# Optimization experiments

Measured on AMD Instinct MI355X. Metric: run time of the kernel, lower is better.

The kernel has to match this reference:

```python
import jax, jax.numpy as jnp
import numpy as np

B, L, D, V, O = 512, 256, 256, 100000, 1000  # L must equal D (see MaxPool1d(kernel_size=D) + squeeze)


def setup_inputs() -> dict:
    key = jax.random.key(0)
    k1, k2, k3, k4, k5 = jax.random.split(key, 5)
    input_sentence = jax.random.randint(k1, (B, L), 0, V)
    emb_weight = jax.random.normal(k2, (V, D), dtype=jnp.float32) * 0.02
    # xavier_uniform for W_b: bound = sqrt(6/(D+D))
    bound = float(np.sqrt(6.0 / (D + D)))
    W_b = jax.random.uniform(k3, (D, D), dtype=jnp.float32, minval=-bound, maxval=bound)
    lw = float(np.sqrt(1.0 / D))
    lin_w = jax.random.uniform(k4, (O, D), dtype=jnp.float32, minval=-lw, maxval=lw)
    lin_b = jax.random.uniform(k5, (O,), dtype=jnp.float32, minval=-lw, maxval=lw)
    return {"input_sentence": input_sentence, "emb_weight": emb_weight,
            "W_b": W_b, "lin_w": lin_w, "lin_b": lin_b}


def reference(input_sentence, emb_weight, W_b, lin_w, lin_b):
    # Embedding lookup: [B, L, D]
    we = emb_weight[input_sentence]
    # torch stores embeddings as [B, D, L] then re-transposes inside the co-attention;
    # net effect: C = tanh(E W_b E^T) with E = [B, L, D]  ->  C: [B, L, L]
    C = jnp.tanh(jnp.einsum('bld,de,bme->blm', we, W_b, we))
    # Dropout(p=0.5) is identity in eval mode.
    # MaxPool1d(kernel_size=D) over last axis with L == D -> max over last dim, keepdims
    max_cow = jnp.max(C, axis=-1, keepdims=True)          # [B, L, 1]
    a_q = jax.nn.softmax(max_cow, axis=1)                  # softmax over L
    # bmm(a_q^T [B,1,L], E [B,L,D]) -> [B,1,D], then squeeze dim 1
    f_w = jnp.einsum('blo,bld->bod', a_q, we)[:, 0, :]     # [B, D]
    return f_w @ lin_w.T + lin_b                           # [B, O]
```

## Files before the change

### kernel.cpp

```cpp
#include <hip/hip_runtime.h>
#include <hip/hip_bf16.h>
#include <math.h>

#define B_ 512
#define L_ 256
#define D_ 256
#define V_ 100000
#define O_ 1000

typedef __attribute__((ext_vector_type(8))) short short8;
typedef __attribute__((ext_vector_type(4))) float f32x4;

static __device__ __forceinline__ unsigned short f2bf(float f) {
    union { float f; unsigned u; } v; v.f = f;
    unsigned r = v.u + 0x7FFFu + ((v.u >> 16) & 1u);
    return (unsigned short)(r >> 16);
}
static __device__ __forceinline__ float bf2f(unsigned short u) {
    union { unsigned u; float f; } v; v.u = ((unsigned)u) << 16;
    return v.f;
}
static __device__ __forceinline__ short8 pack8(float4 a, float4 c) {
    short8 o;
    o[0] = (short)f2bf(a.x); o[1] = (short)f2bf(a.y);
    o[2] = (short)f2bf(a.z); o[3] = (short)f2bf(a.w);
    o[4] = (short)f2bf(c.x); o[5] = (short)f2bf(c.y);
    o[6] = (short)f2bf(c.z); o[7] = (short)f2bf(c.w);
    return o;
}
static __device__ __forceinline__ int fsw(int d) { return d ^ (((d >> 5) & 7) << 2); }

__global__ __launch_bounds__(256) void k_wt(const float* __restrict__ Wb,
                                            unsigned short* __restrict__ Wbf) {
    int i = blockIdx.x * 256 + threadIdx.x;
    Wbf[i] = f2bf(Wb[i]);
}

__global__ __launch_bounds__(512) void k_attn(const int* __restrict__ tok,
                                              const float* __restrict__ emb,
                                              const unsigned short* __restrict__ Wbf,
                                              float* __restrict__ fw) {
    __shared__ __align__(16) char lds[163840];
    char* EsC = lds;
    float* red2    = (float*)(lds + 131072);
    float* scratch = (float*)(lds + 132096);
    float* fred    = (float*)(lds + 132160);

    int b = blockIdx.x;
    int tid = threadIdx.x;
    int wid = tid >> 6, ln = tid & 63;
    int l16 = ln & 15, gp = ln >> 4;
    bool prod = (wid < 4);
    int i0 = (prod ? wid : (wid - 4)) * 64;
    const int* tb = tok + (b << 8);

#pragma unroll
    for (int it = 0; it < 4; it++) {
        int c = it * 512 + tid;
        int row = c >> 5, c16 = c & 31;
        const float4* src = (const float4*)(emb + ((size_t)tb[row] << 8) + (c16 << 3));
        short8 o = pack8(src[0], src[1]);
        *(short8*)(EsC + ((row << 9) | ((c16 << 4) ^ ((row & 7) << 4)))) = o;
    }
    __syncthreads();

    short8 afr[8][4];
    if (prod) {
#pragma unroll
        for (int k = 0; k < 8; k++)
#pragma unroll
            for (int rf = 0; rf < 4; rf++)
                afr[k][rf] = *(const short8*)(Wbf + ((i0 + rf * 16 + l16) << 8) + k * 32 + gp * 8);
    }

    float rmax[16];
#pragma unroll
    for (int i = 0; i < 16; i++) rmax[i] = -1e30f;

    auto P2body = [&](char* HtR) {
        f32x4 acc[4][2] = {};
#pragma unroll
        for (int k0 = 0; k0 < 256; k0 += 32) {
            int kk2 = (k0 + gp * 8) * 2;
            short8 b2[2];
#pragma unroll
            for (int cf = 0; cf < 2; cf++) {
                int m = cf * 16 + l16;
                b2[cf] = *(const short8*)(HtR + ((m << 9) | (kk2 ^ ((m & 7) << 4))));
            }
            int ks = k0 >> 5;
            __builtin_amdgcn_s_setprio(1);
#pragma unroll
            for (int rf = 0; rf < 4; rf++)
#pragma unroll
                for (int cf = 0; cf < 2; cf++)
                    acc[rf][cf] = __builtin_amdgcn_mfma_f32_16x16x32_bf16(
                        afr[ks][rf], b2[cf], acc[rf][cf], 0, 0, 0);
            __builtin_amdgcn_s_setprio(0);
        }
#pragma unroll
        for (int rf = 0; rf < 4; rf++)
#pragma unroll
            for (int r = 0; r < 4; r++)
                rmax[rf * 4 + r] = fmaxf(rmax[rf * 4 + r],
                                         fmaxf(acc[rf][0][r], acc[rf][1][r]));
    };

    for (int s = 0; s < 8; s++) {
        if (prod) {
            char* HtW = lds + 131072 + ((s & 1) << 14);
            f32x4 acc[4][2] = {};
#pragma unroll
            for (int k0 = 0; k0 < 256; k0 += 32) {
                int kk2 = (k0 + gp * 8) * 2;
                short8 b1[2];
#pragma unroll
                for (int cf = 0; cf < 2; cf++) {
                    int jg = s * 32 + cf * 16 + l16;
                    b1[cf] = *(const short8*)(EsC + ((jg << 9) | (kk2 ^ ((jg & 7) << 4))));
                }
                int ks = k0 >> 5;
                __builtin_amdgcn_s_setprio(1);
#pragma unroll
                for (int rf = 0; rf < 4; rf++)
#pragma unroll
                    for (int cf = 0; cf < 2; cf++)
                        acc[rf][cf] = __builtin_amdgcn_mfma_f32_16x16x32_bf16(
                            afr[ks][rf], b1[cf], acc[rf][cf], 0, 0, 0);
                __builtin_amdgcn_s_setprio(0);
            }
#pragma unroll
            for (int rf = 0; rf < 4; rf++)
#pragma unroll
                for (int cf = 0; cf < 2; cf++) {
                    int i = i0 + rf * 16 + gp * 4;
                    int jl = cf * 16 + l16;
                    unsigned long long pk;
                    unsigned short* p = (unsigned short*)&pk;
                    p[0] = f2bf(acc[rf][cf][0]);
                    p[1] = f2bf(acc[rf][cf][1]);
                    p[2] = f2bf(acc[rf][cf][2]);
                    p[3] = f2bf(acc[rf][cf][3]);
                    *(unsigned long long*)(HtW + ((jl << 9) | ((i * 2) ^ ((jl & 7) << 4)))) = pk;
                }
        } else {
            if (s == 0) {
                if (wid > 4) {
#pragma unroll 4
                    for (int it = 0; it < 32; it++) {
                        int ch = it * 64 + ln;
                        int rl = ch >> 5, c16 = ch & 31;
                        int row = i0 + rl;
                        const float4* src = (const float4*)(emb + ((size_t)tb[row] << 8) + (c16 << 3));
                        short8 o = pack8(src[0], src[1]);
                        *(short8*)(EsC + ((row << 9) | ((c16 << 4) ^ ((row & 7) << 4)))) = o;
                    }
                }
#pragma unroll
                for (int k = 0; k < 8; k++)
#pragma unroll
                    for (int rf = 0; rf < 4; rf++) {
                        int l = i0 + rf * 16 + l16;
                        afr[k][rf] = *(const short8*)(EsC +
                            ((l << 9) | ((k * 64 + gp * 16) ^ ((l & 7) << 4))));
                    }
            } else {
                P2body(lds + 131072 + (((s - 1) & 1) << 14));
            }
        }
        __syncthreads();
    }

    if (!prod) {
        P2body(lds + 131072 + (1 << 14));
#pragma unroll
        for (int i = 0; i < 16; i++) {
            float v = rmax[i];
            v = fmaxf(v, __shfl_xor(v, 1));
            v = fmaxf(v, __shfl_xor(v, 2));
            v = fmaxf(v, __shfl_xor(v, 4));
            v = fmaxf(v, __shfl_xor(v, 8));
            rmax[i] = v;
        }
        if (l16 == 0) {
#pragma unroll
            for (int rf = 0; rf < 4; rf++)
#pragma unroll
                for (int r = 0; r < 4; r++)
                    red2[i0 + rf * 16 + gp * 4 + r] = rmax[rf * 4 + r];
        }
    }
    __syncthreads();

    float x = -1e30f;
    if (tid < 256) x = tanhf(red2[tid]);
    float mx = x;
#pragma unroll
    for (int s = 1; s < 64; s <<= 1) mx = fmaxf(mx, __shfl_xor(mx, s));
    if (ln == 0) scratch[wid] = mx;
    __syncthreads();
    float bm = scratch[0];
#pragma unroll
    for (int i = 1; i < 8; i++) bm = fmaxf(bm, scratch[i]);
    float e = (tid < 256) ? expf(x - bm) : 0.f;
    float sm = e;
#pragma unroll
    for (int s = 1; s < 64; s <<= 1) sm += __shfl_xor(sm, s);
    if (ln == 0) scratch[8 + wid] = sm;
    __syncthreads();
    float tot = 0.f;
#pragma unroll
    for (int i = 0; i < 8; i++) tot += scratch[8 + i];
    if (tid < 256) red2[tid] = e / tot;
    __syncthreads();

    {
        int g = tid >> 5;
        int d0 = (tid & 31) << 3;
        float s0[8] = {0.f, 0.f, 0.f, 0.f, 0.f, 0.f, 0.f, 0.f};
        int lbase = g << 4;
#pragma unroll
        for (int li = 0; li < 16; li++) {
            int l = lbase + li;
            float aql = red2[l];
            int byt = (l << 9) | ((d0 * 2) ^ ((l & 7) << 4));
            short8 v = *(const short8*)(EsC + byt);
#pragma unroll
            for (int jj = 0; jj < 8; jj++)
                s0[jj] += aql * bf2f((unsigned short)v[jj]);
        }
        f32x4 w0, w1;
        w0[0] = s0[0]; w0[1] = s0[1]; w0[2] = s0[2]; w0[3] = s0[3];
        w1[0] = s0[4]; w1[1] = s0[5]; w1[2] = s0[6]; w1[3] = s0[7];
        *(f32x4*)(fred + g * 256 + fsw(d0)) = w0;
        *(f32x4*)(fred + g * 256 + fsw(d0 + 4)) = w1;
    }
    __syncthreads();
    if (tid < 256) {
        float f = 0.f;
        int dw = fsw(tid);
#pragma unroll
        for (int g2 = 0; g2 < 16; g2++) f += fred[g2 * 256 + dw];
        fw[(b << 8) + tid] = f;
    }
}

__global__ __launch_bounds__(256) void k_out(const float* __restrict__ fw,
                                             const float* __restrict__ lw,
                                             const float* __restrict__ lb,
                                             float* __restrict__ out) {
    __shared__ float BsT[256][68];
    __shared__ float As[32][260];
    int tid = threadIdx.x;
    int tx = tid & 15, ty = tid >> 4;
    int r0 = blockIdx.y * 32, n0 = blockIdx.x * 64;
#pragma unroll
    for (int it = 0; it < 8; it++) {
        int f4 = it * 256 + tid;
        int i = f4 >> 6, kc = (f4 & 63) << 2;
        *(float4*)&As[i][kc] = *(const float4*)&fw[(r0 + i) * 256 + kc];
    }
#pragma unroll
    for (int it = 0; it < 16; it++) {
        int f4 = it * 256 + tid;
        int n = f4 >> 6, kc = (f4 & 63) << 2;
        int nn = n0 + n;
        float4 v = {0.f, 0.f, 0.f, 0.f};
        if (nn < O_) v = *(const float4*)&lw[(size_t)nn * 256 + kc];
        BsT[kc][n] = v.x; BsT[kc + 1][n] = v.y; BsT[kc + 2][n] = v.z; BsT[kc + 3][n] = v.w;
    }
    __syncthreads();
    float acc[2][4] = {};
#pragma unroll 4
    for (int k = 0; k < 256; k++) {
        float4 bv = *(const float4*)&BsT[k][tx * 4];
        float a0 = As[ty * 2][k], a1 = As[ty * 2 + 1][k];
        acc[0][0] += a0 * bv.x; acc[0][1] += a0 * bv.y; acc[0][2] += a0 * bv.z; acc[0][3] += a0 * bv.w;
        acc[1][0] += a1 * bv.x; acc[1][1] += a1 * bv.y; acc[1][2] += a1 * bv.z; acc[1][3] += a1 * bv.w;
    }
#pragma unroll
    for (int i = 0; i < 2; i++)
#pragma unroll
        for (int j = 0; j < 4; j++) {
            int n = n0 + tx * 4 + j;
            if (n < O_) out[(size_t)(r0 + ty * 2 + i) * O_ + n] = acc[i][j] + lb[n];
        }
}

extern "C" void kernel_launch(void* const* d_in, const int* in_sizes, int n_in,
                              void* d_out, int out_size, void* d_ws, size_t ws_size,
                              hipStream_t stream) {
    const int* tok = (const int*)d_in[0];
    const float* emb = (const float*)d_in[1];
    const float* Wb = (const float*)d_in[2];
    const float* lw = (const float*)d_in[3];
    const float* lb = (const float*)d_in[4];
    float* out = (float*)d_out;

    char* ws = (char*)d_ws;
    unsigned short* Wbf = (unsigned short*)(ws);
    float*          fwp = (float*)(ws + 131072);

    hipLaunchKernelGGL(k_wt,   dim3(256),    dim3(256), 0, stream, Wb, Wbf);
    hipLaunchKernelGGL(k_attn, dim3(512),    dim3(512), 0, stream, tok, emb, Wbf, fwp);
    hipLaunchKernelGGL(k_out,  dim3(16, 16), dim3(256), 0, stream, fwp, lw, lb, out);
}
```

Measured before the change: 79.22 us.

## Restructure attention GEMMs with 32x32 MFMA and register-resident intermediate

Replaces the producer/consumer warp split, which staged the intermediate E·W product through double-buffered LDS, with a scheme where each warp computes its own 32 rows of the intermediate using 32x32x16 MFMAs. The result is converted to bf16 with a packed convert instruction and rearranged across lanes via shuffles so it feeds the second GEMM directly from registers. W_b is pre-transposed and read straight from global/L2 per k-step, and LDS use is trimmed so two blocks can fit per CU. The risks are higher register pressure from the 8 f32x16 accumulators plus 16 B fragments, and repeated global reads of W_b.

```diff
diff --git a/kernel.cpp b/kernel.cpp
--- a/kernel.cpp
+++ b/kernel.cpp
@@ -10,6 +10,7 @@
 
 typedef __attribute__((ext_vector_type(8))) short short8;
 typedef __attribute__((ext_vector_type(4))) float f32x4;
+typedef __attribute__((ext_vector_type(16))) float f32x16;
 
 static __device__ __forceinline__ unsigned short f2bf(float f) {
     union { float f; unsigned u; } v; v.f = f;
@@ -28,19 +29,25 @@
     o[6] = (short)f2bf(c.z); o[7] = (short)f2bf(c.w);
     return o;
 }
+static __device__ __forceinline__ unsigned cvtpk(float lo, float hi) {
+    unsigned r;
+    asm("v_cvt_pk_bf16_f32 %0, %1, %2" : "=v"(r) : "v"(lo), "v"(hi));
+    return r;
+}
 static __device__ __forceinline__ int fsw(int d) { return d ^ (((d >> 5) & 7) << 2); }
 
-__global__ __launch_bounds__(256) void k_wt(const float* __restrict__ Wb,
-                                            unsigned short* __restrict__ Wbf) {
+__global__ __launch_bounds__(256) void k_wtT(const float* __restrict__ Wb,
+                                             unsigned short* __restrict__ Wbt) {
     int i = blockIdx.x * 256 + threadIdx.x;
-    Wbf[i] = f2bf(Wb[i]);
-}
-
-__global__ __launch_bounds__(512) void k_attn(const int* __restrict__ tok,
-                                              const float* __restrict__ emb,
-                                              const unsigned short* __restrict__ Wbf,
-                                              float* __restrict__ fw) {
-    __shared__ __align__(16) char lds[163840];
+    int e = i >> 8, d = i & 255;
+    Wbt[i] = f2bf(Wb[d * 256 + e]);
+}
+
+__global__ __launch_bounds__(512, 2) void k_attn(const int* __restrict__ tok,
+                                                 const float* __restrict__ emb,
+                                                 const unsigned short* __restrict__ Wbt,
+                                                 float* __restrict__ fw) {
+    __shared__ __align__(16) char lds[148544];
     char* EsC = lds;
     float* red2    = (float*)(lds + 131072);
     float* scratch = (float*)(lds + 132096);
@@ -49,147 +56,76 @@
     int b = blockIdx.x;
     int tid = threadIdx.x;
     int wid = tid >> 6, ln = tid & 63;
-    int l16 = ln & 15, gp = ln >> 4;
-    bool prod = (wid < 4);
-    int i0 = (prod ? wid : (wid - 4)) * 64;
+    int l32 = ln & 31, hi = ln >> 5;
+    int r0 = wid << 5;
     const int* tb = tok + (b << 8);
 
-#pragma unroll
-    for (int it = 0; it < 4; it++) {
-        int c = it * 512 + tid;
-        int row = c >> 5, c16 = c & 31;
+#pragma unroll 4
+    for (int it = 0; it < 16; it++) {
+        int g = it * 64 + ln;
+        int row = r0 + (g >> 5), c16 = g & 31;
         const float4* src = (const float4*)(emb + ((size_t)tb[row] << 8) + (c16 << 3));
         short8 o = pack8(src[0], src[1]);
-        *(short8*)(EsC + ((row << 9) | ((c16 << 4) ^ ((row & 7) << 4)))) = o;
-    }
-    __syncthreads();
-
-    short8 afr[8][4];
-    if (prod) {
-#pragma unroll
-        for (int k = 0; k < 8; k++)
-#pragma unroll
-            for (int rf = 0; rf < 4; rf++)
-                afr[k][rf] = *(const short8*)(Wbf + ((i0 + rf * 16 + l16) << 8) + k * 32 + gp * 8);
-    }
-
-    float rmax[16];
-#pragma unroll
-    for (int i = 0; i < 16; i++) rmax[i] = -1e30f;
-
-    auto P2body = [&](char* HtR) {
-        f32x4 acc[4][2] = {};
-#pragma unroll
-        for (int k0 = 0; k0 < 256; k0 += 32) {
-            int kk2 = (k0 + gp * 8) * 2;
-            short8 b2[2];
-#pragma unroll
-            for (int cf = 0; cf < 2; cf++) {
-                int m = cf * 16 + l16;
-                b2[cf] = *(const short8*)(HtR + ((m << 9) | (kk2 ^ ((m & 7) << 4))));
+        *(short8*)(EsC + ((row << 9) | ((c16 << 4) ^ ((row & 15) << 4)))) = o;
+    }
+
+    f32x16 acc1[8] = {};
+    {
+        int rr = r0 + l32;
+        int rsw = (rr & 15) << 4;
+#pragma unroll 2
+        for (int ks = 0; ks < 16; ks++) {
+            short8 b1 = *(const short8*)(EsC +
+                ((rr << 9) | (((ks << 5) + (hi << 4)) ^ rsw)));
+#pragma unroll
+            for (int t = 0; t < 8; t++) {
+                short8 a = *(const short8*)(Wbt + (((t << 5) + l32) << 8) + (ks << 4) + (hi << 3));
+                acc1[t] = __builtin_amdgcn_mfma_f32_32x32x16_bf16(a, b1, acc1[t], 0, 0, 0);
             }
-            int ks = k0 >> 5;
-            __builtin_amdgcn_s_setprio(1);
-#pragma unroll
-            for (int rf = 0; rf < 4; rf++)
-#pragma unroll
-                for (int cf = 0; cf < 2; cf++)
-                    acc[rf][cf] = __builtin_amdgcn_mfma_f32_16x16x32_bf16(
-                        afr[ks][rf], b2[cf], acc[rf][cf], 0, 0, 0);
-            __builtin_amdgcn_s_setprio(0);
-        }
-#pragma unroll
-        for (int rf = 0; rf < 4; rf++)
-#pragma unroll
-            for (int r = 0; r < 4; r++)
-                rmax[rf * 4 + r] = fmaxf(rmax[rf * 4 + r],
-                                         fmaxf(acc[rf][0][r], acc[rf][1][r]));
-    };
-
-    for (int s = 0; s < 8; s++) {
-        if (prod) {
-            char* HtW = lds + 131072 + ((s & 1) << 14);
-            f32x4 acc[4][2] = {};
-#pragma unroll
-            for (int k0 = 0; k0 < 256; k0 += 32) {
-                int kk2 = (k0 + gp * 8) * 2;
-                short8 b1[2];
-#pragma unroll
-                for (int cf = 0; cf < 2; cf++) {
-                    int jg = s * 32 + cf * 16 + l16;
-                    b1[cf] = *(const short8*)(EsC + ((jg << 9) | (kk2 ^ ((jg & 7) << 4))));
-                }
-                int ks = k0 >> 5;
-                __builtin_amdgcn_s_setprio(1);
-#pragma unroll
-                for (int rf = 0; rf < 4; rf++)
-#pragma unroll
-                    for (int cf = 0; cf < 2; cf++)
-                        acc[rf][cf] = __builtin_amdgcn_mfma_f32_16x16x32_bf16(
-                            afr[ks][rf], b1[cf], acc[rf][cf], 0, 0, 0);
-                __builtin_amdgcn_s_setprio(0);
-            }
-#pragma unroll
-            for (int rf = 0; rf < 4; rf++)
-#pragma unroll
-                for (int cf = 0; cf < 2; cf++) {
-                    int i = i0 + rf * 16 + gp * 4;
-                    int jl = cf * 16 + l16;
-                    unsigned long long pk;
-                    unsigned short* p = (unsigned short*)&pk;
-                    p[0] = f2bf(acc[rf][cf][0]);
-                    p[1] = f2bf(acc[rf][cf][1]);
-                    p[2] = f2bf(acc[rf][cf][2]);
-                    p[3] = f2bf(acc[rf][cf][3]);
-                    *(unsigned long long*)(HtW + ((jl << 9) | ((i * 2) ^ ((jl & 7) << 4)))) = pk;
-                }
-        } else {
-            if (s == 0) {
-                if (wid > 4) {
-#pragma unroll 4
-                    for (int it = 0; it < 32; it++) {
-                        int ch = it * 64 + ln;
-                        int rl = ch >> 5, c16 = ch & 31;
-                        int row = i0 + rl;
-                        const float4* src = (const float4*)(emb + ((size_t)tb[row] << 8) + (c16 << 3));
-                        short8 o = pack8(src[0], src[1]);
-                        *(short8*)(EsC + ((row << 9) | ((c16 << 4) ^ ((row & 7) << 4)))) = o;
-                    }
-                }
-#pragma unroll
-                for (int k = 0; k < 8; k++)
-#pragma unroll
-                    for (int rf = 0; rf < 4; rf++) {
-                        int l = i0 + rf * 16 + l16;
-                        afr[k][rf] = *(const short8*)(EsC +
-                            ((l << 9) | ((k * 64 + gp * 16) ^ ((l & 7) << 4))));
-                    }
-            } else {
-                P2body(lds + 131072 + (((s - 1) & 1) << 14));
-            }
-        }
-        __syncthreads();
-    }
-
-    if (!prod) {
-        P2body(lds + 131072 + (1 << 14));
-#pragma unroll
-        for (int i = 0; i < 16; i++) {
-            float v = rmax[i];
-            v = fmaxf(v, __shfl_xor(v, 1));
-            v = fmaxf(v, __shfl_xor(v, 2));
-            v = fmaxf(v, __shfl_xor(v, 4));
-            v = fmaxf(v, __shfl_xor(v, 8));
-            rmax[i] = v;
-        }
-        if (l16 == 0) {
-#pragma unroll
-            for (int rf = 0; rf < 4; rf++)
-#pragma unroll
-                for (int r = 0; r < 4; r++)
-                    red2[i0 + rf * 16 + gp * 4 + r] = rmax[rf * 4 + r];
-        }
-    }
+        }
+    }
+
+    short8 b2[16];
+#pragma unroll
+    for (int ks = 0; ks < 16; ks++) {
+        int t = ks >> 1, base = (ks & 1) << 3;
+        unsigned u0 = cvtpk(acc1[t][base + 0], acc1[t][base + 1]);
+        unsigned u1 = cvtpk(acc1[t][base + 2], acc1[t][base + 3]);
+        unsigned u2 = cvtpk(acc1[t][base + 4], acc1[t][base + 5]);
+        unsigned u3 = cvtpk(acc1[t][base + 6], acc1[t][base + 7]);
+        unsigned su0 = __shfl_xor(u0, 32);
+        unsigned su1 = __shfl_xor(u1, 32);
+        unsigned su2 = __shfl_xor(u2, 32);
+        unsigned su3 = __shfl_xor(u3, 32);
+        union { unsigned u[4]; short8 s; } w;
+        w.u[0] = hi ? su2 : u0;
+        w.u[1] = hi ? su3 : u1;
+        w.u[2] = hi ? u2 : su0;
+        w.u[3] = hi ? u3 : su1;
+        b2[ks] = w.s;
+    }
+
+    __syncthreads();
+
+    float rmax1 = -1e30f;
+    for (int mt = 0; mt < 8; mt += 2) {
+        f32x16 aA = {}, aB = {};
+        int rrA = (mt << 5) + l32, rrB = rrA + 32;
+        int swA = (rrA & 15) << 4, swB = (rrB & 15) << 4;
+#pragma unroll
+        for (int ks = 0; ks < 16; ks++) {
+            int cc = (ks << 5) + (hi << 4);
+            short8 xA = *(const short8*)(EsC + ((rrA << 9) | (cc ^ swA)));
+            short8 xB = *(const short8*)(EsC + ((rrB << 9) | (cc ^ swB)));
+            aA = __builtin_amdgcn_mfma_f32_32x32x16_bf16(xA, b2[ks], aA, 0, 0, 0);
+            aB = __builtin_amdgcn_mfma_f32_32x32x16_bf16(xB, b2[ks], aB, 0, 0, 0);
+        }
+#pragma unroll
+        for (int r = 0; r < 16; r++)
+            rmax1 = fmaxf(rmax1, fmaxf(aA[r], aB[r]));
+    }
+    rmax1 = fmaxf(rmax1, __shfl_xor(rmax1, 32));
+    if (hi == 0) red2[r0 + l32] = rmax1;
     __syncthreads();
 
     float x = -1e30f;
@@ -223,7 +159,7 @@
         for (int li = 0; li < 16; li++) {
             int l = lbase + li;
             float aql = red2[l];
-            int byt = (l << 9) | ((d0 * 2) ^ ((l & 7) << 4));
+            int byt = (l << 9) | ((d0 * 2) ^ ((l & 15) << 4));
             short8 v = *(const short8*)(EsC + byt);
 #pragma unroll
             for (int jj = 0; jj < 8; jj++)
@@ -298,10 +234,10 @@
     float* out = (float*)d_out;
 
     char* ws = (char*)d_ws;
-    unsigned short* Wbf = (unsigned short*)(ws);
+    unsigned short* Wbt = (unsigned short*)(ws);
     float*          fwp = (float*)(ws + 131072);
 
-    hipLaunchKernelGGL(k_wt,   dim3(256),    dim3(256), 0, stream, Wb, Wbf);
-    hipLaunchKernelGGL(k_attn, dim3(512),    dim3(512), 0, stream, tok, emb, Wbf, fwp);
+    hipLaunchKernelGGL(k_wtT,  dim3(256),    dim3(256), 0, stream, Wb, Wbt);
+    hipLaunchKernelGGL(k_attn, dim3(512),    dim3(512), 0, stream, tok, emb, Wbt, fwp);
     hipLaunchKernelGGL(k_out,  dim3(16, 16), dim3(256), 0, stream, fwp, lw, lb, out);
 }
```

Result: slower. 112.4 us (+41.8%).
